# Performance work log

Hardware: AMD Instinct MI355X
Metric: run time of the kernel (lower is better)

## Reference

```python
import jax, jax.numpy as jnp
import numpy as np

NUM_EMBEDDINGS = 8192
EMBEDDING_DIM = 256
COMMITMENT_COST = 0.25


def setup_inputs() -> dict:
    key = jax.random.key(0)
    k1, k2 = jax.random.split(key)
    z_e = jax.random.normal(k1, (16, 2048, EMBEDDING_DIM), dtype=jnp.float32)
    # nn.Embedding init: uniform(-1/K, 1/K)
    codebook = jax.random.uniform(
        k2, (NUM_EMBEDDINGS, EMBEDDING_DIM), dtype=jnp.float32,
        minval=-1.0 / NUM_EMBEDDINGS, maxval=1.0 / NUM_EMBEDDINGS)
    return {"z_e": z_e, "codebook": codebook}


def _nearest_indices(z_flat, codebook):
    # squared euclidean distances; argmin is identical to argmin of cdist
    # z_flat: [T, D], codebook: [K, D] -> dist2: [T, K]
    x2 = jnp.sum(z_flat * z_flat, axis=-1, keepdims=True)          # [T, 1]
    w2 = jnp.sum(codebook * codebook, axis=-1)                      # [K]
    xw = jnp.einsum('td,kd->tk', z_flat, codebook)                  # [T, K]
    dist2 = x2 - 2.0 * xw + w2
    return jnp.argmin(dist2, axis=1)                                # [T]


def reference(z_e, codebook):
    original_shape = z_e.shape
    z_e_flat = z_e.reshape(-1, EMBEDDING_DIM)
    indices = _nearest_indices(z_e_flat, codebook)
    z_q = codebook[indices].reshape(original_shape)
    # straight-through estimator
    z_q_ste = z_e + jax.lax.stop_gradient(z_q - z_e)
    commitment_loss = jnp.mean((z_e - jax.lax.stop_gradient(z_q_ste)) ** 2)
    codebook_loss = jnp.mean((z_q_ste - jax.lax.stop_gradient(z_e)) ** 2)
    loss = codebook_loss + COMMITMENT_COST * commitment_loss
    # codebook usage: fraction of unique indices (jit-friendly via scatter)
    used = jnp.zeros((NUM_EMBEDDINGS,), dtype=jnp.float32).at[indices].set(1.0)
    usage = jnp.sum(used) / NUM_EMBEDDINGS
    return (z_q_ste, loss, usage)
```

## Files before the change

kernel.cpp:

```cpp
#include <hip/hip_runtime.h>
#include <float.h>

#define T_TOTAL 32768
#define KC      8192
#define DIM     256

#define LOSS_IDX  ((size_t)T_TOTAL * DIM)
#define USAGE_IDX (LOSS_IDX + 1)

typedef short s16x8 __attribute__((ext_vector_type(8)));
typedef float f32x4 __attribute__((ext_vector_type(4)));

#define WS_W2    0
#define WS_FLAGS 32768
#define WS_CBF   65536

__device__ __forceinline__ unsigned short f2bf(float f) {
    unsigned int u = __float_as_uint(f);
    u += 0x7FFFu + ((u >> 16) & 1u);
    return (unsigned short)(u >> 16);
}

__global__ __launch_bounds__(256) void vq_prep(const float* __restrict__ cb,
                                               unsigned short* __restrict__ cbb,
                                               float* __restrict__ w2,
                                               int* __restrict__ flags,
                                               float* __restrict__ out) {
    const int blk = blockIdx.x, tid = threadIdx.x;
    size_t i = (size_t)blk * 2048 + (size_t)tid * 8;
    float4 a = *(const float4*)(cb + i);
    float4 b = *(const float4*)(cb + i + 4);
    uint4 o;
    o.x = (unsigned)f2bf(a.x) | ((unsigned)f2bf(a.y) << 16);
    o.y = (unsigned)f2bf(a.z) | ((unsigned)f2bf(a.w) << 16);
    o.z = (unsigned)f2bf(b.x) | ((unsigned)f2bf(b.y) << 16);
    o.w = (unsigned)f2bf(b.z) | ((unsigned)f2bf(b.w) << 16);
    *(uint4*)(cbb + i) = o;
    float s = a.x * a.x + a.y * a.y + a.z * a.z + a.w * a.w
            + b.x * b.x + b.y * b.y + b.z * b.z + b.w * b.w;
    #pragma unroll
    for (int m = 1; m <= 16; m <<= 1) s += __shfl_xor(s, m);
    if ((tid & 31) == 0) w2[blk * 8 + (tid >> 5)] = s;
    if (blk < 32) flags[blk * 256 + tid] = 0;
    if (blk == 0 && tid == 0) { out[LOSS_IDX] = 0.0f; out[USAGE_IDX] = 0.0f; }
}

__global__ __launch_bounds__(512, 2) void vq_main(const unsigned short* __restrict__ cbb,
                                                  const float* __restrict__ w2g,
                                                  const float* __restrict__ z_e,
                                                  const float* __restrict__ cb,
                                                  float* __restrict__ out,
                                                  int* __restrict__ flags) {
    __shared__ unsigned short ca[8][4][2048];
    __shared__ unsigned long long smin[128];
    __shared__ float wls[8];

    const int tid  = threadIdx.x;
    const int lane = tid & 63;
    const int w    = tid >> 6;
    const int wr   = w >> 2;
    const int wc   = w & 3;
    const int quad = lane >> 4;
    const int l15  = lane & 15;
    const int t0   = blockIdx.x * 128;

    if (tid < 128) smin[tid] = ~0ULL;
    __syncthreads();

    const int srow = lane >> 3;
    const int ssl  = lane & 7;
    const unsigned short* pstage = cbb + (wc * 32 + srow) * DIM + (ssl ^ srow) * 8;

    #define STAGE(PC, KW, BP)                                                           \
        {                                                                               \
            _Pragma("unroll")                                                           \
            for (int q = 0; q < 4; ++q) {                                               \
                __builtin_amdgcn_global_load_lds(                                       \
                    (const __attribute__((address_space(1))) void*)((PC) + (KW) * 64 + q * 2048), \
                    (__attribute__((address_space(3))) void*)(&ca[w][BP][q * 512]),     \
                    16, 0, 0);                                                          \
            }                                                                           \
        }

    const unsigned short* fragp[4];
    #pragma unroll
    for (int kk = 0; kk < 2; ++kk)
        #pragma unroll
        for (int j = 0; j < 2; ++j) {
            int row = j * 16 + l15;
            int sl = (kk * 4 + quad) ^ (l15 & 7);
            fragp[kk * 2 + j] = &ca[w][0][row * 64 + sl * 8];
        }

    #define READFRAGS(FB, BP)                                                           \
        {                                                                               \
            _Pragma("unroll")                                                           \
            for (int f = 0; f < 4; ++f)                                                 \
                (FB)[f] = *(const s16x8*)(fragp[f] + (BP) * 2048);                      \
        }

    STAGE(pstage, 0, 0); STAGE(pstage, 1, 1); STAGE(pstage, 2, 2); STAGE(pstage, 3, 3);
    s16x8 af[4][8];
    #pragma unroll
    for (int i = 0; i < 4; ++i) {
        #pragma unroll
        for (int ks = 0; ks < 8; ++ks) {
            const float* p = z_e + (size_t)(t0 + wr * 64 + i * 16 + l15) * DIM + ks * 32 + quad * 8;
            float4 a = *(const float4*)p;
            float4 b = *(const float4*)(p + 4);
            s16x8 v;
            v[0] = (short)f2bf(a.x); v[1] = (short)f2bf(a.y);
            v[2] = (short)f2bf(a.z); v[3] = (short)f2bf(a.w);
            v[4] = (short)f2bf(b.x); v[5] = (short)f2bf(b.y);
            v[6] = (short)f2bf(b.z); v[7] = (short)f2bf(b.w);
            af[i][ks] = v;
        }
    }

    float best[4][4];
    int   bidx[4][4];
    #pragma unroll
    for (int i = 0; i < 4; ++i)
        #pragma unroll
        for (int r = 0; r < 4; ++r) { best[i][r] = FLT_MAX; bidx[i][r] = 0x7FFFFFFF; }

    const float* pw2 = w2g + wc * 32 + l15;

    s16x8 regB[2][4];
    __builtin_amdgcn_s_waitcnt(0x0F7C);
    READFRAGS(regB[0], 0);

    for (int c = 0; c < 64; ++c) {
        f32x4 acc[4][2];
        #pragma unroll
        for (int i = 0; i < 4; ++i)
            #pragma unroll
            for (int j = 0; j < 2; ++j) acc[i][j] = (f32x4){0.f, 0.f, 0.f, 0.f};

        const unsigned short* pcn = pstage + ((size_t)((c + 1) & 63) << 15);

        #pragma unroll
        for (int kw = 0; kw < 4; ++kw) {
            __builtin_amdgcn_s_waitcnt(0xC07F);
            STAGE(pcn, kw, kw);
            __builtin_amdgcn_s_waitcnt(0x0F78);
            READFRAGS(regB[(kw + 1) & 1], (kw + 1) & 3);
            const s16x8* cur = regB[kw & 1];
            __builtin_amdgcn_s_setprio(1);
            #pragma unroll
            for (int kk = 0; kk < 2; ++kk)
                #pragma unroll
                for (int i = 0; i < 4; ++i)
                    #pragma unroll
                    for (int j = 0; j < 2; ++j)
                        acc[i][j] = __builtin_amdgcn_mfma_f32_16x16x32_bf16(af[i][kw * 2 + kk], cur[kk * 2 + j], acc[i][j], 0, 0, 0);
            __builtin_amdgcn_s_setprio(0);
        }

        #pragma unroll
        for (int j = 0; j < 2; ++j) {
            int col = c * 128 + wc * 32 + j * 16 + l15;
            float w2v = pw2[c * 128 + j * 16];
            #pragma unroll
            for (int i = 0; i < 4; ++i)
                #pragma unroll
                for (int r = 0; r < 4; ++r) {
                    float s = fmaf(-2.0f, acc[i][j][r], w2v);
                    if (s < best[i][r]) { best[i][r] = s; bidx[i][r] = col; }
                }
        }
    }

    #pragma unroll
    for (int i = 0; i < 4; ++i)
        #pragma unroll
        for (int r = 0; r < 4; ++r) {
            float b = best[i][r]; int ix = bidx[i][r];
            #pragma unroll
            for (int m = 1; m < 16; m <<= 1) {
                float ob = __shfl_xor(b, m);
                int   oi = __shfl_xor(ix, m);
                if (ob < b || (ob == b && oi < ix)) { b = ob; ix = oi; }
            }
            if (l15 == 0) {
                unsigned int fb = __float_as_uint(b);
                fb = (fb & 0x80000000u) ? ~fb : (fb | 0x80000000u);
                unsigned long long key = ((unsigned long long)fb << 32) | (unsigned int)ix;
                atomicMin(&smin[wr * 64 + i * 16 + quad * 4 + r], key);
            }
        }
    __syncthreads();

    float lsum = 0.0f;
    for (int t = w * 16; t < w * 16 + 16; ++t) {
        int tok = t0 + t;
        int k = (int)(unsigned int)(smin[t] & 0xFFFFFFFFull);
        if (lane == 0) flags[k] = 1;
        float4 cv = *(const float4*)(cb + (size_t)k * DIM + lane * 4);
        float4 zv = *(const float4*)(z_e + (size_t)tok * DIM + lane * 4);
        float dx = zv.x - cv.x, dy = zv.y - cv.y, dz = zv.z - cv.z, dw = zv.w - cv.w;
        lsum += dx * dx + dy * dy + dz * dz + dw * dw;
        *(float4*)(out + (size_t)tok * DIM + lane * 4) = cv;
    }
    #pragma unroll
    for (int m = 32; m >= 1; m >>= 1) lsum += __shfl_xor(lsum, m);
    if (lane == 0) wls[w] = lsum;
    __syncthreads();
    if (tid == 0) {
        float bsum = 0.0f;
        #pragma unroll
        for (int q = 0; q < 8; ++q) bsum += wls[q];
        atomicAdd(out + LOSS_IDX, bsum * (1.25f / (float)LOSS_IDX));
    }
}

__global__ __launch_bounds__(256) void vq_usage(const int* __restrict__ flags,
                                                float* __restrict__ out) {
    __shared__ int ws[4];
    int tid = threadIdx.x;
    int s = 0;
    for (int i = tid; i < KC; i += 256) s += flags[i];
    #pragma unroll
    for (int m = 32; m >= 1; m >>= 1) s += __shfl_xor(s, m);
    if ((tid & 63) == 0) ws[tid >> 6] = s;
    __syncthreads();
    if (tid == 0) out[USAGE_IDX] = (float)(ws[0] + ws[1] + ws[2] + ws[3]) / (float)KC;
}

extern "C" void kernel_launch(void* const* d_in, const int* in_sizes, int n_in,
                              void* d_out, int out_size, void* d_ws, size_t ws_size,
                              hipStream_t stream) {
    (void)in_sizes; (void)n_in; (void)out_size; (void)ws_size;
    const float* z_e = (const float*)d_in[0];
    const float* cb  = (const float*)d_in[1];
    float* out = (float*)d_out;

    char* ws = (char*)d_ws;
    float* w2    = (float*)(ws + WS_W2);
    int*   flags = (int*)(ws + WS_FLAGS);
    unsigned short* cbb = (unsigned short*)(ws + WS_CBF);

    vq_prep<<<KC / 8, 256, 0, stream>>>(cb, cbb, w2, flags, out);
    vq_main<<<T_TOTAL / 128, 512, 0, stream>>>(cbb, w2, z_e, cb, out, flags);
    vq_usage<<<1, 256, 0, stream>>>(flags, out);
}
```

Baseline: 243.1 us.

## Split codebook across blocks with 512-token tiles and global atomicMin argmin

Each block now handles 512 tokens (one 64-token strip per wave) against a quarter of the codebook, instead of 128 tokens against the full codebook. Every staged codebook tile is therefore reused by all eight waves over more tokens, which cuts codebook traffic per token. The per-token argmin is merged across the four codebook-quarter blocks with a 64-bit atomicMin into the output buffer, which the prep kernel initialises. A new gather kernel then writes the selected codebook rows, the loss and the usage flags. This adds an extra launch, global atomics and a round trip through the output buffer.

```diff
diff --git a/kernel.cpp b/kernel.cpp
--- a/kernel.cpp
+++ b/kernel.cpp
@@ -42,34 +42,32 @@
     for (int m = 1; m <= 16; m <<= 1) s += __shfl_xor(s, m);
     if ((tid & 31) == 0) w2[blk * 8 + (tid >> 5)] = s;
     if (blk < 32) flags[blk * 256 + tid] = 0;
+    if (blk < 128) {
+        int t = blk * 256 + tid;
+        *(unsigned long long*)(out + ((size_t)t << 8)) = ~0ULL;
+    }
     if (blk == 0 && tid == 0) { out[LOSS_IDX] = 0.0f; out[USAGE_IDX] = 0.0f; }
 }
 
 __global__ __launch_bounds__(512, 2) void vq_main(const unsigned short* __restrict__ cbb,
                                                   const float* __restrict__ w2g,
                                                   const float* __restrict__ z_e,
-                                                  const float* __restrict__ cb,
-                                                  float* __restrict__ out,
-                                                  int* __restrict__ flags) {
+                                                  float* __restrict__ out) {
     __shared__ unsigned short ca[8][4][2048];
-    __shared__ unsigned long long smin[128];
-    __shared__ float wls[8];
 
     const int tid  = threadIdx.x;
     const int lane = tid & 63;
     const int w    = tid >> 6;
-    const int wr   = w >> 2;
-    const int wc   = w & 3;
     const int quad = lane >> 4;
     const int l15  = lane & 15;
-    const int t0   = blockIdx.x * 128;
-
-    if (tid < 128) smin[tid] = ~0ULL;
-    __syncthreads();
+    const int tb   = blockIdx.x >> 2;
+    const int cq   = blockIdx.x & 3;
+    const int t0   = tb * 512;
+    const int cbase = cq * 2048;
 
     const int srow = lane >> 3;
     const int ssl  = lane & 7;
-    const unsigned short* pstage = cbb + (wc * 32 + srow) * DIM + (ssl ^ srow) * 8;
+    const unsigned short* pstage = cbb + (size_t)(cbase + srow) * DIM + (ssl ^ srow) * 8;
 
     #define STAGE(PC, KW, BP)                                                           \
         {                                                                               \
@@ -105,7 +103,7 @@
     for (int i = 0; i < 4; ++i) {
         #pragma unroll
         for (int ks = 0; ks < 8; ++ks) {
-            const float* p = z_e + (size_t)(t0 + wr * 64 + i * 16 + l15) * DIM + ks * 32 + quad * 8;
+            const float* p = z_e + (size_t)(t0 + w * 64 + i * 16 + l15) * DIM + ks * 32 + quad * 8;
             float4 a = *(const float4*)p;
             float4 b = *(const float4*)(p + 4);
             s16x8 v;
@@ -124,7 +122,7 @@
         #pragma unroll
         for (int r = 0; r < 4; ++r) { best[i][r] = FLT_MAX; bidx[i][r] = 0x7FFFFFFF; }
 
-    const float* pw2 = w2g + wc * 32 + l15;
+    const float* pw2 = w2g + cbase + l15;
 
     s16x8 regB[2][4];
     __builtin_amdgcn_s_waitcnt(0x0F7C);
@@ -137,7 +135,7 @@
             #pragma unroll
             for (int j = 0; j < 2; ++j) acc[i][j] = (f32x4){0.f, 0.f, 0.f, 0.f};
 
-        const unsigned short* pcn = pstage + ((size_t)((c + 1) & 63) << 15);
+        const unsigned short* pcn = pstage + ((size_t)((c + 1) & 63) << 13);
 
         #pragma unroll
         for (int kw = 0; kw < 4; ++kw) {
@@ -159,8 +157,8 @@
 
         #pragma unroll
         for (int j = 0; j < 2; ++j) {
-            int col = c * 128 + wc * 32 + j * 16 + l15;
-            float w2v = pw2[c * 128 + j * 16];
+            int col = cbase + c * 32 + j * 16 + l15;
+            float w2v = pw2[c * 32 + j * 16];
             #pragma unroll
             for (int i = 0; i < 4; ++i)
                 #pragma unroll
@@ -186,30 +184,40 @@
                 unsigned int fb = __float_as_uint(b);
                 fb = (fb & 0x80000000u) ? ~fb : (fb | 0x80000000u);
                 unsigned long long key = ((unsigned long long)fb << 32) | (unsigned int)ix;
-                atomicMin(&smin[wr * 64 + i * 16 + quad * 4 + r], key);
+                int tok = t0 + w * 64 + i * 16 + quad * 4 + r;
+                atomicMin((unsigned long long*)(out + ((size_t)tok << 8)), key);
             }
         }
-    __syncthreads();
+}
+
+__global__ __launch_bounds__(256) void vq_gather(const float* __restrict__ cb,
+                                                 const float* __restrict__ z_e,
+                                                 float* __restrict__ out,
+                                                 int* __restrict__ flags) {
+    __shared__ float wls[4];
+    const int tid  = threadIdx.x;
+    const int lane = tid & 63;
+    const int w    = tid >> 6;
+    const int t0   = blockIdx.x * 128;
 
     float lsum = 0.0f;
-    for (int t = w * 16; t < w * 16 + 16; ++t) {
+    for (int t = w * 32; t < w * 32 + 32; ++t) {
         int tok = t0 + t;
-        int k = (int)(unsigned int)(smin[t] & 0xFFFFFFFFull);
+        unsigned long long key = *(const unsigned long long*)(out + ((size_t)tok << 8));
+        int k = (int)(unsigned int)(key & 0xFFFFFFFFull);
         if (lane == 0) flags[k] = 1;
         float4 cv = *(const float4*)(cb + (size_t)k * DIM + lane * 4);
         float4 zv = *(const float4*)(z_e + (size_t)tok * DIM + lane * 4);
         float dx = zv.x - cv.x, dy = zv.y - cv.y, dz = zv.z - cv.z, dw = zv.w - cv.w;
         lsum += dx * dx + dy * dy + dz * dz + dw * dw;
-        *(float4*)(out + (size_t)tok * DIM + lane * 4) = cv;
+        *(float4*)(out + ((size_t)tok << 8) + lane * 4) = cv;
     }
     #pragma unroll
     for (int m = 32; m >= 1; m >>= 1) lsum += __shfl_xor(lsum, m);
     if (lane == 0) wls[w] = lsum;
     __syncthreads();
     if (tid == 0) {
-        float bsum = 0.0f;
-        #pragma unroll
-        for (int q = 0; q < 8; ++q) bsum += wls[q];
+        float bsum = wls[0] + wls[1] + wls[2] + wls[3];
         atomicAdd(out + LOSS_IDX, bsum * (1.25f / (float)LOSS_IDX));
     }
 }
@@ -241,6 +249,7 @@
     unsigned short* cbb = (unsigned short*)(ws + WS_CBF);
 
     vq_prep<<<KC / 8, 256, 0, stream>>>(cb, cbb, w2, flags, out);
-    vq_main<<<T_TOTAL / 128, 512, 0, stream>>>(cbb, w2, z_e, cb, out, flags);
+    vq_main<<<256, 512, 0, stream>>>(cbb, w2, z_e, out);
+    vq_gather<<<T_TOTAL / 128, 256, 0, stream>>>(cb, z_e, out, flags);
     vq_usage<<<1, 256, 0, stream>>>(flags, out);
 }
```

After: 261.0 us. +7.3%, slower.
